# Kernel tuning notes

Hardware: AMD Instinct MI355X
Metric: run time of the kernel (lower is better)

The kernel has to match this reference:

```python
import jax, jax.numpy as jnp
import numpy as np

NUM_QUBIT = 20
NUM_LAYERS = 4
DIM = 2 ** NUM_QUBIT

# constant CNOT (control kind gate: apply X on target when control=1)
_CNOT = jnp.array([[1, 0, 0, 0],
                   [0, 1, 0, 0],
                   [0, 0, 0, 1],
                   [0, 0, 1, 0]], dtype=jnp.complex64)


def _ry(t):
    # hf0 for a parameterized single-qubit rotation gate Ry(theta)
    c = jnp.cos(t / 2)
    s = jnp.sin(t / 2)
    return jnp.stack([jnp.stack([c, -s]), jnp.stack([s, c])]).astype(jnp.complex64)


def _apply_1q(state, u2, q):
    # state: (2,)*n complex; contract gate on qubit axis q (numqi.sim.state.apply_gate)
    out = jnp.tensordot(u2, state, axes=((1,), (q,)))
    return jnp.moveaxis(out, 0, q)


def _apply_2q(state, u4, q0, q1):
    # 4x4 two-qubit gate on axes (q0, q1) (covers apply_control_n_gate for CNOT)
    out = jnp.tensordot(u4.reshape(2, 2, 2, 2), state, axes=((2, 3), (q0, q1)))
    return jnp.moveaxis(out, (0, 1), (q0, q1))


def setup_inputs() -> dict:
    key = jax.random.key(0)
    k1, k2, k3 = jax.random.split(key, 3)
    theta = jax.random.normal(k1, (NUM_LAYERS, NUM_QUBIT), dtype=jnp.float32)
    qr = jax.random.normal(k2, (DIM,), dtype=jnp.float32)
    qi = jax.random.normal(k3, (DIM,), dtype=jnp.float32)
    # normalize initial state vector
    nrm = jnp.sqrt(jnp.sum(qr * qr + qi * qi))
    return {"theta": theta, "q0_real": qr / nrm, "q0_imag": qi / nrm}


def reference(theta, q0_real, q0_imag):
    # forward of _CircuitFunction: sequential gate application on the state vector
    state = (q0_real.astype(jnp.complex64) + 1j * q0_imag.astype(jnp.complex64))
    state = state.reshape((2,) * NUM_QUBIT)
    for layer in range(NUM_LAYERS):
        for q in range(NUM_QUBIT):          # parameterized 'unitary' gates
            state = _apply_1q(state, _ry(theta[layer, q]), q)
        for q in range(NUM_QUBIT - 1):      # constant 'control' gates (CNOT chain)
            state = _apply_2q(state, _CNOT, q, q + 1)
    flat = state.reshape(DIM)
    # return real/imag stacked so output dtype is real float32
    return jnp.stack([jnp.real(flat), jnp.imag(flat)])
```

## Files before the change

### kernel.cpp

```cpp
#include <hip/hip_runtime.h>
#include <cstdint>

#define NQ 20
#define DIM (1u << NQ)

typedef float f32x2 __attribute__((ext_vector_type(2)));
typedef float f32x4 __attribute__((ext_vector_type(4)));

constexpr unsigned cpair_mask(int l, int b) {
    unsigned m = 1u << b;
    for (int k = 0; k < l; ++k) m ^= m >> 1;
    return m;
}
constexpr unsigned cginv1(unsigned x) {
    x ^= x >> 1; x ^= x >> 2; x ^= x >> 4; x ^= x >> 8; x ^= x >> 16;
    return x & 0xFFFFFu;
}
constexpr unsigned csel_mask(int l, int b) {
    unsigned R = 0;
    for (int k = 0; k < NQ; ++k) {
        unsigned w = 1u << k;
        for (int t = 0; t < l; ++t) w = cginv1(w);
        if ((w >> b) & 1u) R |= 1u << k;
    }
    return R;
}
constexpr unsigned cswz(unsigned t) { return t ^ ((t >> 5) & 0xFu); }

struct GateC { unsigned R; unsigned sb; int valid; int tix; int thix; };
struct GroupC { int pv[2]; unsigned gxs[4]; unsigned lgxs[4]; GateC gt[3]; unsigned m01[2]; };
struct SchedC { GroupC g[20]; int bar[20]; int ng; };
struct PhC { SchedC s; int FL, GAP; };

constexpr unsigned to_local(unsigned m, int FL, int GAP) {
    return (m & ((1u << FL) - 1u)) | ((m >> (FL + GAP)) << FL);
}

constexpr void addg(SchedC& s, int FL, int GAP, int bar,
                    int l0, int b0, int l1, int b1, int l2, int b2) {
    GroupC g{};
    int ls[3] = {l0, l1, l2}; int bs[3] = {b0, b1, b2};
    unsigned m[2] = {0, 0};
    for (int j = 0; j < 3; ++j) {
        bool val = ls[j] >= 0;
        if (j < 2) m[j] = val ? cpair_mask(ls[j], bs[j]) : (1u << bs[j]);
        g.gt[j].R = val ? csel_mask(ls[j], bs[j]) : 0u;
        g.gt[j].valid = val ? 1 : 0;
        g.gt[j].tix = val ? (ls[j] * NQ + bs[j]) : 0;
        g.gt[j].thix = val ? (ls[j] * NQ + (NQ - 1 - bs[j])) : 0;
    }
    g.m01[0] = m[0]; g.m01[1] = m[1];
    for (int e = 0; e < 4; ++e) {
        unsigned x = ((e & 1) ? m[0] : 0u) ^ ((e & 2) ? m[1] : 0u);
        g.gxs[e] = x;
        g.lgxs[e] = to_local(x, FL, GAP);
    }
    for (int j = 0; j < 3; ++j) {
        unsigned sb = 0;
        for (int e = 0; e < 4; ++e)
            if (__builtin_popcount(g.gxs[e] & g.gt[j].R) & 1) sb |= (1u << e);
        g.gt[j].sb = sb;
    }
    int pv[2] = {0, 0};
    for (int j = 0; j < 2; ++j) {
        unsigned lm = to_local(m[j], FL, GAP);
        int p = 0; for (int k = 0; k < 12; ++k) if ((lm >> k) & 1) p = k;
        pv[j] = p;
    }
    if (pv[0] > pv[1]) { int t = pv[0]; pv[0] = pv[1]; pv[1] = t; }
    g.pv[0] = pv[0]; g.pv[1] = pv[1];
    s.bar[s.ng] = bar;
    s.g[s.ng] = g; s.ng++;
}

constexpr PhC mk_phase(int ph) {
    PhC P{};
    if (ph == 0) {
        P.FL = 12; P.GAP = 8;
        addg(P.s, 12, 8, 0, 0,0, 0,1, -1,0);
        addg(P.s, 12, 8, 1, 0,2, 0,3, -1,0);
        addg(P.s, 12, 8, 0, 0,4, 0,5, -1,0);
        addg(P.s, 12, 8, 0, 0,6, 0,7, -1,0);
        addg(P.s, 12, 8, 1, 0,8, 0,9, -1,0);
        addg(P.s, 12, 8, 1, 0,10, 0,11, -1,0);
    } else if (ph == 1) {
        P.FL = 4; P.GAP = 8;
        addg(P.s, 4, 8, 0, 0,12, 0,13, -1,0);
        addg(P.s, 4, 8, 1, 0,14, 0,15, -1,0);
        addg(P.s, 4, 8, 1, 0,16, 0,17, -1,0);
        addg(P.s, 4, 8, 1, 0,18, 0,19, 1,19);
        addg(P.s, 4, 8, 1, 1,13, 1,14, -1,0);
        addg(P.s, 4, 8, 1, 1,15, 1,16, -1,0);
        addg(P.s, 4, 8, 1, 1,17, 1,18, 2,18);
        addg(P.s, 4, 8, 1, 2,14, 2,15, -1,0);
        addg(P.s, 4, 8, 1, 2,19, -1,0, -1,0);
        addg(P.s, 4, 8, 1, 2,16, 2,17, 3,17);
        addg(P.s, 4, 8, 1, 3,15, 3,16, -1,0);
        addg(P.s, 4, 8, 1, 3,18, 3,19, -1,0);
    } else if (ph == 2) {
        P.FL = 6; P.GAP = 3;
        addg(P.s, 6, 3, 0, 1,11, 1,12, 2,12);
        addg(P.s, 6, 3, 1, 1,10, 2,11, -1,0);
        addg(P.s, 6, 3, 1, 2,13, 3,12, -1,0);
        addg(P.s, 6, 3, 1, 3,13, 3,14, -1,0);
    } else {
        P.FL = 12; P.GAP = 8;
        addg(P.s, 12, 8, 0, 1,0, 1,1, -1,0);
        addg(P.s, 12, 8, 1, 1,2, 1,3, -1,0);
        addg(P.s, 12, 8, 0, 1,4, 1,5, -1,0);
        addg(P.s, 12, 8, 0, 1,6, 1,7, -1,0);
        addg(P.s, 12, 8, 1, 1,8, 1,9, 2,9);
        addg(P.s, 12, 8, 1, 2,0, 2,1, -1,0);
        addg(P.s, 12, 8, 0, 2,2, 2,3, -1,0);
        addg(P.s, 12, 8, 0, 2,4, 2,5, -1,0);
        addg(P.s, 12, 8, 0, 2,6, 2,7, -1,0);
        addg(P.s, 12, 8, 1, 2,8, 2,10, -1,0);
        addg(P.s, 12, 8, 1, 3,2, 3,3, -1,0);
        addg(P.s, 12, 8, 0, 3,4, 3,5, -1,0);
        addg(P.s, 12, 8, 0, 3,6, 3,7, -1,0);
        addg(P.s, 12, 8, 1, 3,8, 3,9, -1,0);
        addg(P.s, 12, 8, 1, 3,10, 3,11, -1,0);
        addg(P.s, 12, 8, 1, 3,0, 3,1, -1,0);
    }
    return P;
}

constexpr bool pivots_ok(int ph) {
    PhC P = mk_phase(ph);
    for (int i = 0; i < P.s.ng; ++i)
        if (P.s.g[i].pv[0] == P.s.g[i].pv[1]) return false;
    return true;
}
constexpr bool window_ok(int ph) {
    PhC P = mk_phase(ph);
    for (int i = 0; i < P.s.ng; ++i)
        for (int e = 0; e < 4; ++e) {
            unsigned lm = P.s.g[i].lgxs[e];
            unsigned inv = (lm & ((1u << P.FL) - 1u)) | ((lm >> P.FL) << (P.FL + P.GAP));
            if (inv != P.s.g[i].gxs[e]) return false;
        }
    return true;
}
constexpr bool triples_ok(int ph) {
    PhC P = mk_phase(ph);
    for (int i = 0; i < P.s.ng; ++i)
        if (P.s.g[i].gt[2].valid) {
            int l = P.s.g[i].gt[2].tix / NQ, b = P.s.g[i].gt[2].tix % NQ;
            if (cpair_mask(l, b) != (P.s.g[i].m01[0] ^ P.s.g[i].m01[1])) return false;
        }
    return true;
}
constexpr bool order_ok() {
    int el[96] = {}, eb[96] = {}; int n = 0;
    for (int ph = 0; ph < 4; ++ph) {
        PhC P = mk_phase(ph);
        for (int gi = 0; gi < P.s.ng; ++gi)
            for (int j = 0; j < 3; ++j)
                if (P.s.g[gi].gt[j].valid) {
                    el[n] = P.s.g[gi].gt[j].tix / NQ;
                    eb[n] = P.s.g[gi].gt[j].tix % NQ;
                    ++n;
                }
    }
    if (n != 80) return false;
    bool seen[80] = {};
    unsigned M[80] = {}, R[80] = {};
    for (int i = 0; i < n; ++i) {
        int idx = el[i] * NQ + eb[i];
        if (seen[idx]) return false;
        seen[idx] = true;
        M[i] = cpair_mask(el[i], eb[i]);
        R[i] = csel_mask(el[i], eb[i]);
    }
    for (int i = 0; i < n; ++i)
        for (int j = i + 1; j < n; ++j)
            if (el[i] > el[j]) {
                int p1 = __builtin_popcount(M[i] & R[j]) & 1;
                int p2 = __builtin_popcount(M[j] & R[i]) & 1;
                if (p1 != p2) return false;
            }
    return true;
}
static_assert(pivots_ok(0) && pivots_ok(1) && pivots_ok(2) && pivots_ok(3),
              "pivot collision: coset decomposition not bijective");
static_assert(window_ok(0) && window_ok(1) && window_ok(2) && window_ok(3),
              "gate mask outside phase window");
static_assert(triples_ok(0) && triples_ok(1) && triples_ok(2) && triples_ok(3),
              "third gate mask != m0^m1");
static_assert(order_ok(), "executed gate order not circuit-equivalent");

constexpr unsigned max_gxs(const GroupC& g) {
    unsigned m = 0;
    for (int e = 0; e < 4; ++e) if (g.gxs[e] > m) m = g.gxs[e];
    return m;
}

__device__ __forceinline__ unsigned swz(unsigned t) { return t ^ ((t >> 5) & 0xFu); }
__device__ __forceinline__ f32x2 splat2(float x) { f32x2 r = {x, x}; return r; }

template<int FL, int GAP>
__device__ __forceinline__ unsigned gmapF(unsigned t, unsigned mid) {
    if constexpr (FL == 12) return (mid << 12) | t;
    else return (t & ((1u << FL) - 1u)) | ((mid & ((1u << GAP) - 1u)) << FL)
              | ((t >> FL) << (FL + GAP)) | ((mid >> GAP) << (GAP + 12));
}

__device__ __forceinline__ unsigned expand2(unsigned u, int p0, int p1) {
    u = ((u >> p0) << (p0 + 1)) | (u & ((1u << p0) - 1u));
    u = ((u >> p1) << (p1 + 1)) | (u & ((1u << p1) - 1u));
    return u;
}

#define APPLY_GROUP(G, v, g0, cd, sd)                                           \
    {                                                                            \
        _Pragma("unroll")                                                        \
        for (int j = 0; j < 3; ++j) {                                            \
            if ((G).gt[j].valid) {                                               \
                const f32x2 cc_ = splat2((cd)[j]);                               \
                const unsigned par_ = (unsigned)__popc((g0) & (G).gt[j].R) & 1u; \
                const float sp_ = par_ ? (sd)[j] : -(sd)[j];                     \
                const int xr_ = (j == 0) ? 1 : ((j == 1) ? 2 : 3);               \
                _Pragma("unroll")                                                \
                for (int pr = 0; pr < 2; ++pr) {                                 \
                    const int ea = (j == 0) ? (pr << 1) : pr;                    \
                    const int eb = ea ^ xr_;                                     \
                    const f32x2 sg_ = splat2((((G).gt[j].sb >> ea) & 1u) ? -sp_ : sp_); \
                    const f32x2 a_ = v[ea], b_ = v[eb];                          \
                    v[ea] = cc_ * a_ + sg_ * b_;                                 \
                    v[eb] = cc_ * b_ - sg_ * a_;                                 \
                }                                                                \
            }                                                                    \
        }                                                                        \
    }

template<int PH, bool IS_INIT, bool IS_FINAL>
__global__ __launch_bounds__(1024) void k_phase(f32x2* __restrict__ st,
                                                const float* __restrict__ qr,
                                                const float* __restrict__ qi,
                                                const float* __restrict__ theta,
                                                float* __restrict__ out) {
    constexpr PhC P = mk_phase(PH);
    constexpr int FL = P.FL, GAP = P.GAP, NG = P.s.ng;
    __shared__ __align__(16) f32x2 lds[4096];
    __shared__ float2 trigS[80];
    const unsigned tid = threadIdx.x;
    const unsigned mid = blockIdx.x;

    if (tid < 80) {
        int l = tid / NQ, b = tid % NQ;
        float th = 0.5f * theta[l * NQ + (NQ - 1 - b)];
        trigS[tid] = make_float2(cosf(th), sinf(th));
    }

    {
        constexpr GroupC G = P.s.g[0];
        constexpr bool CIN = (max_gxs(G) < 4u);
        const unsigned t0 = expand2(tid, G.pv[0], G.pv[1]);
        const unsigned g0 = gmapF<FL, GAP>(t0, mid);
        f32x2 v[4];
        if constexpr (IS_INIT) {
            const f32x4* r4 = reinterpret_cast<const f32x4*>(qr);
            const f32x4* i4 = reinterpret_cast<const f32x4*>(qi);
            f32x4 ra = r4[g0 >> 2], ia = i4[g0 >> 2];
            const float re[4] = {ra.x, ra.y, ra.z, ra.w};
            const float im[4] = {ia.x, ia.y, ia.z, ia.w};
#pragma unroll
            for (int e = 0; e < 4; ++e) v[e] = f32x2{re[G.gxs[e] & 3u], im[G.gxs[e] & 3u]};
        } else if constexpr (CIN) {
            const f32x4* s4 = reinterpret_cast<const f32x4*>(st);
            f32x4 q[2];
            q[0] = s4[g0 >> 1]; q[1] = s4[(g0 >> 1) + 1];
            const float* qq = reinterpret_cast<const float*>(q);
#pragma unroll
            for (int e = 0; e < 4; ++e) {
                const unsigned j = G.gxs[e] & 3u;
                v[e] = f32x2{qq[2 * j], qq[2 * j + 1]};
            }
        } else {
#pragma unroll
            for (int e = 0; e < 4; ++e) v[e] = st[g0 ^ G.gxs[e]];
        }
        float cd[3], sd[3];
#pragma unroll
        for (int j = 0; j < 3; ++j)
            if (G.gt[j].valid) {
                float th = 0.5f * theta[G.gt[j].thix];
                cd[j] = cosf(th); sd[j] = sinf(th);
            }
        APPLY_GROUP(G, v, g0, cd, sd);
#pragma unroll
        for (int e = 0; e < 4; ++e) lds[swz(t0 ^ G.lgxs[e])] = v[e];
    }

#pragma unroll
    for (int gi = 1; gi < NG - 1; ++gi) {
        if (P.s.bar[gi]) __syncthreads();
        else __builtin_amdgcn_wave_barrier();
        const unsigned t0 = expand2(tid, P.s.g[gi].pv[0], P.s.g[gi].pv[1]);
        const unsigned g0 = gmapF<FL, GAP>(t0, mid);
        const unsigned sz0 = swz(t0);
        f32x2 v[4]; unsigned ad[4];
#pragma unroll
        for (int e = 0; e < 4; ++e) {
            ad[e] = sz0 ^ cswz(P.s.g[gi].lgxs[e]);
            v[e] = lds[ad[e]];
        }
        float cd[3], sd[3];
#pragma unroll
        for (int j = 0; j < 3; ++j)
            if (P.s.g[gi].gt[j].valid) {
                float2 cs = trigS[P.s.g[gi].gt[j].tix];
                cd[j] = cs.x; sd[j] = cs.y;
            }
        APPLY_GROUP(P.s.g[gi], v, g0, cd, sd);
#pragma unroll
        for (int e = 0; e < 4; ++e) lds[ad[e]] = v[e];
    }

    __syncthreads();

    {
        constexpr GroupC G = P.s.g[NG - 1];
        const unsigned t0 = expand2(tid, G.pv[0], G.pv[1]);
        const unsigned g0 = gmapF<FL, GAP>(t0, mid);
        f32x2 v[4];
#pragma unroll
        for (int e = 0; e < 4; ++e) v[e] = lds[swz(t0 ^ G.lgxs[e])];
        float cd[3], sd[3];
#pragma unroll
        for (int j = 0; j < 3; ++j)
            if (G.gt[j].valid) {
                float2 cs = trigS[G.gt[j].tix];
                cd[j] = cs.x; sd[j] = cs.y;
            }
        APPLY_GROUP(G, v, g0, cd, sd);
        if constexpr (IS_FINAL) {
            const unsigned i0 = g0 ^ (g0 >> 4) ^ (g0 >> 8) ^ (g0 >> 12) ^ (g0 >> 16);
            const unsigned base = i0 & ~3u;
            const unsigned lo = i0 & 3u;
            f32x2 u[4];
#pragma unroll
            for (int e = 0; e < 4; ++e) u[G.gxs[e] & 3u] = v[e];
#pragma unroll
            for (int bit = 1; bit <= 2; bit <<= 1) {
                const bool c = (lo & (unsigned)bit) != 0u;
                f32x2 t[4];
#pragma unroll
                for (int k = 0; k < 4; ++k) t[k] = c ? u[k ^ bit] : u[k];
#pragma unroll
                for (int k = 0; k < 4; ++k) u[k] = t[k];
            }
            float4* oR = reinterpret_cast<float4*>(out + base);
            float4* oI = reinterpret_cast<float4*>(out + DIM + base);
            oR[0] = make_float4(u[0].x, u[1].x, u[2].x, u[3].x);
            oI[0] = make_float4(u[0].y, u[1].y, u[2].y, u[3].y);
        } else {
#pragma unroll
            for (int e = 0; e < 4; ++e) st[g0 ^ G.gxs[e]] = v[e];
        }
    }
}

extern "C" void kernel_launch(void* const* d_in, const int* in_sizes, int n_in,
                              void* d_out, int out_size, void* d_ws, size_t ws_size,
                              hipStream_t stream) {
    const float* theta = (const float*)d_in[0];
    const float* qr    = (const float*)d_in[1];
    const float* qi    = (const float*)d_in[2];
    float* out = (float*)d_out;
    f32x2* st = (f32x2*)d_ws;

    k_phase<0, true,  false><<<256, 1024, 0, stream>>>(st, qr, qi, theta, out);
    k_phase<1, false, false><<<256, 1024, 0, stream>>>(st, qr, qi, theta, out);
    k_phase<2, false, false><<<256, 1024, 0, stream>>>(st, qr, qi, theta, out);
    k_phase<3, false, true ><<<256, 1024, 0, stream>>>(st, qr, qi, theta, out);
}
```

Before: 42.16 us.

## Shrink local qubit window to 11 bits and rebalance gate schedule across phases

Reduces each block's local state tile from 4096 to 2048 amplitudes, with 512 threads per block and 512 blocks, and redistributes the gate groups among the four phases to fit the new window layout. The aim is to give the 256-CU GPU at least one block per CU and to lower the LDS per block so more blocks can be resident. In exchange, each phase can hold fewer qubits locally, so the gate schedule must be rebuilt. The second-to-last phase now carries more groups, which may cost extra LDS round-trips and barriers.

```diff
diff --git a/kernel.cpp b/kernel.cpp
--- a/kernel.cpp
+++ b/kernel.cpp
@@ -3,6 +3,9 @@
 
 #define NQ 20
 #define DIM (1u << NQ)
+#define NLOC 11
+#define NTHR 512
+#define NGRID 512
 
 typedef float f32x2 __attribute__((ext_vector_type(2)));
 typedef float f32x4 __attribute__((ext_vector_type(4)));
@@ -64,7 +67,7 @@
     int pv[2] = {0, 0};
     for (int j = 0; j < 2; ++j) {
         unsigned lm = to_local(m[j], FL, GAP);
-        int p = 0; for (int k = 0; k < 12; ++k) if ((lm >> k) & 1) p = k;
+        int p = 0; for (int k = 0; k < NLOC; ++k) if ((lm >> k) & 1) p = k;
         pv[j] = p;
     }
     if (pv[0] > pv[1]) { int t = pv[0]; pv[0] = pv[1]; pv[1] = t; }
@@ -76,51 +79,51 @@
 constexpr PhC mk_phase(int ph) {
     PhC P{};
     if (ph == 0) {
-        P.FL = 12; P.GAP = 8;
-        addg(P.s, 12, 8, 0, 0,0, 0,1, -1,0);
-        addg(P.s, 12, 8, 1, 0,2, 0,3, -1,0);
-        addg(P.s, 12, 8, 0, 0,4, 0,5, -1,0);
-        addg(P.s, 12, 8, 0, 0,6, 0,7, -1,0);
-        addg(P.s, 12, 8, 1, 0,8, 0,9, -1,0);
-        addg(P.s, 12, 8, 1, 0,10, 0,11, -1,0);
+        P.FL = NLOC; P.GAP = 9;
+        addg(P.s, NLOC, 9, 0, 0,0, 0,1, -1,0);
+        addg(P.s, NLOC, 9, 1, 0,2, 0,3, -1,0);
+        addg(P.s, NLOC, 9, 0, 0,4, 0,5, -1,0);
+        addg(P.s, NLOC, 9, 0, 0,6, 0,7, -1,0);
+        addg(P.s, NLOC, 9, 1, 0,8, -1,0, -1,0);
+        addg(P.s, NLOC, 9, 1, 0,9, 0,10, -1,0);
     } else if (ph == 1) {
-        P.FL = 4; P.GAP = 8;
-        addg(P.s, 4, 8, 0, 0,12, 0,13, -1,0);
-        addg(P.s, 4, 8, 1, 0,14, 0,15, -1,0);
-        addg(P.s, 4, 8, 1, 0,16, 0,17, -1,0);
-        addg(P.s, 4, 8, 1, 0,18, 0,19, 1,19);
-        addg(P.s, 4, 8, 1, 1,13, 1,14, -1,0);
-        addg(P.s, 4, 8, 1, 1,15, 1,16, -1,0);
-        addg(P.s, 4, 8, 1, 1,17, 1,18, 2,18);
-        addg(P.s, 4, 8, 1, 2,14, 2,15, -1,0);
-        addg(P.s, 4, 8, 1, 2,19, -1,0, -1,0);
-        addg(P.s, 4, 8, 1, 2,16, 2,17, 3,17);
-        addg(P.s, 4, 8, 1, 3,15, 3,16, -1,0);
-        addg(P.s, 4, 8, 1, 3,18, 3,19, -1,0);
+        P.FL = 3; P.GAP = 9;
+        addg(P.s, 3, 9, 0, 0,12, 0,13, -1,0);
+        addg(P.s, 3, 9, 1, 0,14, 0,15, -1,0);
+        addg(P.s, 3, 9, 1, 0,16, 0,17, -1,0);
+        addg(P.s, 3, 9, 1, 0,18, 0,19, 1,19);
+        addg(P.s, 3, 9, 1, 1,13, 1,14, -1,0);
+        addg(P.s, 3, 9, 0, 1,15, 1,16, -1,0);
+        addg(P.s, 3, 9, 1, 1,17, 1,18, 2,18);
+        addg(P.s, 3, 9, 1, 2,14, 2,15, -1,0);
+        addg(P.s, 3, 9, 1, 2,19, -1,0, -1,0);
+        addg(P.s, 3, 9, 1, 2,16, 2,17, 3,17);
+        addg(P.s, 3, 9, 1, 3,15, 3,16, -1,0);
+        addg(P.s, 3, 9, 1, 3,18, 3,19, -1,0);
     } else if (ph == 2) {
-        P.FL = 6; P.GAP = 3;
-        addg(P.s, 6, 3, 0, 1,11, 1,12, 2,12);
-        addg(P.s, 6, 3, 1, 1,10, 2,11, -1,0);
-        addg(P.s, 6, 3, 1, 2,13, 3,12, -1,0);
-        addg(P.s, 6, 3, 1, 3,13, 3,14, -1,0);
+        P.FL = 3; P.GAP = 5;
+        addg(P.s, 3, 5, 0, 0,11, 1,9, -1,0);
+        addg(P.s, 3, 5, 1, 1,11, 1,12, 2,12);
+        addg(P.s, 3, 5, 0, 1,10, 2,11, -1,0);
+        addg(P.s, 3, 5, 1, 2,10, 2,13, -1,0);
+        addg(P.s, 3, 5, 1, 3,11, 3,12, -1,0);
+        addg(P.s, 3, 5, 1, 3,13, 3,14, -1,0);
     } else {
-        P.FL = 12; P.GAP = 8;
-        addg(P.s, 12, 8, 0, 1,0, 1,1, -1,0);
-        addg(P.s, 12, 8, 1, 1,2, 1,3, -1,0);
-        addg(P.s, 12, 8, 0, 1,4, 1,5, -1,0);
-        addg(P.s, 12, 8, 0, 1,6, 1,7, -1,0);
-        addg(P.s, 12, 8, 1, 1,8, 1,9, 2,9);
-        addg(P.s, 12, 8, 1, 2,0, 2,1, -1,0);
-        addg(P.s, 12, 8, 0, 2,2, 2,3, -1,0);
-        addg(P.s, 12, 8, 0, 2,4, 2,5, -1,0);
-        addg(P.s, 12, 8, 0, 2,6, 2,7, -1,0);
-        addg(P.s, 12, 8, 1, 2,8, 2,10, -1,0);
-        addg(P.s, 12, 8, 1, 3,2, 3,3, -1,0);
-        addg(P.s, 12, 8, 0, 3,4, 3,5, -1,0);
-        addg(P.s, 12, 8, 0, 3,6, 3,7, -1,0);
-        addg(P.s, 12, 8, 1, 3,8, 3,9, -1,0);
-        addg(P.s, 12, 8, 1, 3,10, 3,11, -1,0);
-        addg(P.s, 12, 8, 1, 3,0, 3,1, -1,0);
+        P.FL = NLOC; P.GAP = 9;
+        addg(P.s, NLOC, 9, 0, 1,0, 1,1, -1,0);
+        addg(P.s, NLOC, 9, 1, 1,2, 1,3, -1,0);
+        addg(P.s, NLOC, 9, 0, 1,4, 1,5, -1,0);
+        addg(P.s, NLOC, 9, 0, 1,6, 1,7, -1,0);
+        addg(P.s, NLOC, 9, 1, 1,8, -1,0, -1,0);
+        addg(P.s, NLOC, 9, 1, 2,9, 2,0, -1,0);
+        addg(P.s, NLOC, 9, 1, 2,7, 2,8, 3,8);
+        addg(P.s, NLOC, 9, 1, 2,5, 2,6, 3,6);
+        addg(P.s, NLOC, 9, 0, 2,3, 2,4, 3,4);
+        addg(P.s, NLOC, 9, 0, 2,1, 2,2, 3,2);
+        addg(P.s, NLOC, 9, 0, 3,3, 3,5, -1,0);
+        addg(P.s, NLOC, 9, 1, 3,7, 3,9, -1,0);
+        addg(P.s, NLOC, 9, 1, 3,10, -1,0, -1,0);
+        addg(P.s, NLOC, 9, 1, 3,0, 3,1, -1,0);
     }
     return P;
 }
@@ -200,9 +203,9 @@
 
 template<int FL, int GAP>
 __device__ __forceinline__ unsigned gmapF(unsigned t, unsigned mid) {
-    if constexpr (FL == 12) return (mid << 12) | t;
+    if constexpr (FL == NLOC) return (mid << NLOC) | t;
     else return (t & ((1u << FL) - 1u)) | ((mid & ((1u << GAP) - 1u)) << FL)
-              | ((t >> FL) << (FL + GAP)) | ((mid >> GAP) << (GAP + 12));
+              | ((t >> FL) << (FL + GAP)) | ((mid >> GAP) << (GAP + NLOC));
 }
 
 __device__ __forceinline__ unsigned expand2(unsigned u, int p0, int p1) {
@@ -234,14 +237,14 @@
     }
 
 template<int PH, bool IS_INIT, bool IS_FINAL>
-__global__ __launch_bounds__(1024) void k_phase(f32x2* __restrict__ st,
+__global__ __launch_bounds__(NTHR) void k_phase(f32x2* __restrict__ st,
                                                 const float* __restrict__ qr,
                                                 const float* __restrict__ qi,
                                                 const float* __restrict__ theta,
                                                 float* __restrict__ out) {
     constexpr PhC P = mk_phase(PH);
     constexpr int FL = P.FL, GAP = P.GAP, NG = P.s.ng;
-    __shared__ __align__(16) f32x2 lds[4096];
+    __shared__ __align__(16) f32x2 lds[1u << NLOC];
     __shared__ float2 trigS[80];
     const unsigned tid = threadIdx.x;
     const unsigned mid = blockIdx.x;
@@ -370,8 +373,8 @@
     float* out = (float*)d_out;
     f32x2* st = (f32x2*)d_ws;
 
-    k_phase<0, true,  false><<<256, 1024, 0, stream>>>(st, qr, qi, theta, out);
-    k_phase<1, false, false><<<256, 1024, 0, stream>>>(st, qr, qi, theta, out);
-    k_phase<2, false, false><<<256, 1024, 0, stream>>>(st, qr, qi, theta, out);
-    k_phase<3, false, true ><<<256, 1024, 0, stream>>>(st, qr, qi, theta, out);
-}
+    k_phase<0, true,  false><<<NGRID, NTHR, 0, stream>>>(st, qr, qi, theta, out);
+    k_phase<1, false, false><<<NGRID, NTHR, 0, stream>>>(st, qr, qi, theta, out);
+    k_phase<2, false, false><<<NGRID, NTHR, 0, stream>>>(st, qr, qi, theta, out);
+    k_phase<3, false, true ><<<NGRID, NTHR, 0, stream>>>(st, qr, qi, theta, out);
+}
```

After: 46.26 us. +9.7%, slower.
